# Performance work log

Measured on AMD Instinct MI355X. Metric: run time of the kernel, lower is better.

## Reference

```python
import jax, jax.numpy as jnp
import numpy as np

# Static ragged segment lengths (batch index column of `indices` is built to match).
COUNTS = (3072, 4096, 2048, 3584, 2560, 4096, 3072, 2048)
OFFSETS = np.concatenate([[0], np.cumsum(COUNTS)])  # static, jit-safe
N = int(OFFSETS[-1])
C_IN = 256
C_OUT = 256


def setup_inputs() -> dict:
    key = jax.random.key(0)
    kf, kq, kk, kv, kbq, kbk, kbv, kidx = jax.random.split(key, 8)
    features = jax.random.normal(kf, (N, C_IN), dtype=jnp.float32)
    # indices[:,0] = batch id (sorted, ragged counts); remaining cols = spatial coords.
    batch_col = jnp.asarray(np.repeat(np.arange(len(COUNTS)), COUNTS), dtype=jnp.int32)
    spatial = jax.random.randint(kidx, (N, 3), 0, 1024, dtype=jnp.int32)
    indices = jnp.concatenate([batch_col[:, None], spatial], axis=1)
    s = 1.0 / np.sqrt(C_IN)
    Wq = jax.random.normal(kq, (C_OUT, C_IN), dtype=jnp.float32) * s
    Wk = jax.random.normal(kk, (C_OUT, C_IN), dtype=jnp.float32) * s
    Wv = jax.random.normal(kv, (C_OUT, C_IN), dtype=jnp.float32) * s
    bq = jax.random.normal(kbq, (C_OUT,), dtype=jnp.float32) * 0.01
    bk = jax.random.normal(kbk, (C_OUT,), dtype=jnp.float32) * 0.01
    bv = jax.random.normal(kbv, (C_OUT,), dtype=jnp.float32) * 0.01
    return {"features": features, "indices": indices,
            "Wq": Wq, "bq": bq, "Wk": Wk, "bk": bk, "Wv": Wv, "bv": bv}


def reference(features, indices, Wq, bq, Wk, bk, Wv, bv):
    # Linear layers commute with the ragged split, so project once globally.
    q = features @ Wq.T + bq  # [N, C_OUT]
    k = features @ Wk.T + bk
    v = features @ Wv.T + bv
    outs = []
    for i in range(len(COUNTS)):  # small fixed set of ragged segments (static sizes)
        s, e = int(OFFSETS[i]), int(OFFSETS[i + 1])
        qi, ki, vi = q[s:e], k[s:e], v[s:e]  # [n_i, C]
        attn = jax.nn.softmax(qi @ ki.T, axis=-1)  # [n_i, n_i]
        outs.append(attn @ vi)
    return jnp.concatenate(outs, axis=0)  # [N, C_OUT]
```

## Files before the change

### kernel.cpp

```cpp
#include <hip/hip_runtime.h>


typedef _Float16 f16x8 __attribute__((ext_vector_type(8)));
typedef _Float16 f16x4 __attribute__((ext_vector_type(4)));
typedef _Float16 f16x2 __attribute__((ext_vector_type(2)));
typedef float    f32x4 __attribute__((ext_vector_type(4)));
typedef unsigned int u32;

#define MFMA(a,b,c) __builtin_amdgcn_mfma_f32_16x16x32_f16((a),(b),(c),0,0,0)

typedef __attribute__((address_space(1))) const u32 gu32_t;
typedef __attribute__((address_space(3))) u32 lu32_t;

__device__ __forceinline__ void gll16(const void* g, void* l) {
  __builtin_amdgcn_global_load_lds((gu32_t*)g, (lu32_t*)l, 16, 0, 0);
}
#define VMCNT(n) asm volatile("s_waitcnt vmcnt(" #n ")" ::: "memory")
#define BAR() __builtin_amdgcn_s_barrier()

__constant__ int c_off[9] = {0, 3072, 7168, 9216, 12800, 15360, 19456, 22528, 24576};

static constexpr int NTOK = 24576;
static constexpr int C    = 256;

__global__ __launch_bounds__(256) void wsplit_kernel(
    const float* __restrict__ Wq, const float* __restrict__ Wk, const float* __restrict__ Wv,
    _Float16* __restrict__ Whi, _Float16* __restrict__ Wlo)
{
  int idx = blockIdx.x * 256 + threadIdx.x;
  int mat = idx >> 16;
  int r   = idx & 65535;
  const float* W = (mat == 0) ? Wq : (mat == 1) ? Wk : Wv;
  float v = W[r];
  _Float16 h = (_Float16)v;
  Whi[idx] = h;
  Wlo[idx] = (_Float16)(v - (float)h);
}

__global__ __launch_bounds__(256) void proj_kernel(
    const float* __restrict__ X,
    const float* __restrict__ bq, const float* __restrict__ bk, const float* __restrict__ bv,
    const _Float16* __restrict__ Whi, const _Float16* __restrict__ Wlo,
    float* __restrict__ Qf, _Float16* __restrict__ Kh, _Float16* __restrict__ Vt)
{
  __shared__ _Float16 wl[2][2][16][256];

  const int tid  = threadIdx.x;
  const int w    = tid >> 6;
  const int lane = tid & 63;
  const int l15  = lane & 15;
  const int lg   = lane >> 4;
  const int t0   = blockIdx.x * 64 + w * 16;

  f16x8 xhi[8], xlo[8];
  {
    const float* src = X + (size_t)(t0 + l15) * C + lg * 8;
    #pragma unroll
    for (int kk = 0; kk < 8; ++kk) {
      float4 a = *(const float4*)(src + kk * 32);
      float4 b = *(const float4*)(src + kk * 32 + 4);
      float v[8] = {a.x, a.y, a.z, a.w, b.x, b.y, b.z, b.w};
      f16x8 h, l;
      #pragma unroll
      for (int j = 0; j < 8; ++j) {
        _Float16 hi = (_Float16)v[j];
        h[j] = hi;
        l[j] = (_Float16)(v[j] - (float)hi);
      }
      xhi[kk] = h;
      xlo[kk] = l;
    }
  }

  int soff[4];
  const _Float16* sbase[4];
  #pragma unroll
  for (int i = 0; i < 4; ++i) {
    int g = w * 256 + i * 64 + lane;
    int col = (g >> 5) & 15, p = g & 31;
    int c = (p & 24) | ((p ^ col) & 7);
    soff[i] = col * 256 + c * 8;
    sbase[i] = (g >> 9) ? Wlo : Whi;
  }

  int koff[8];
  {
    const int pm = l15 & 7;
    #pragma unroll
    for (int kk = 0; kk < 8; ++kk) {
      int cch = kk * 4 + lg;
      int p = (cch & 24) | ((cch ^ pm) & 7);
      koff[kk] = l15 * 512 + p * 16;
    }
  }

  auto stage = [&](int buf, int j) {
    const int rowbase = (j >> 4) * 256 + (j & 15) * 16;
    char* dst = (char*)&wl[buf][0][0][0] + (w * 256) * 16;
    #pragma unroll
    for (int i = 0; i < 4; ++i)
      gll16(sbase[i] + (size_t)rowbase * 256 + soff[i], dst + i * 1024);
  };

  stage(0, 0);
  stage(1, 1);
  VMCNT(4);
  BAR();

  #pragma unroll 1
  for (int j = 0; j < 48; ++j) {
    const int buf = j & 1;
    const char* bh_base = (const char*)&wl[buf][0][0][0];
    const char* bl_base = (const char*)&wl[buf][1][0][0];
    f32x4 acc = {0.f, 0.f, 0.f, 0.f};
    const int mat = j >> 4;
    if (mat < 2) {
      #pragma unroll
      for (int kk = 0; kk < 8; ++kk) {
        f16x8 bh = *(const f16x8*)(bh_base + koff[kk]);
        f16x8 bl = *(const f16x8*)(bl_base + koff[kk]);
        acc = MFMA(xhi[kk], bh, acc);
        acc = MFMA(xlo[kk], bh, acc);
        acc = MFMA(xhi[kk], bl, acc);
      }
    } else {
      #pragma unroll
      for (int kk = 0; kk < 8; ++kk) {
        f16x8 bh = *(const f16x8*)(bh_base + koff[kk]);
        acc = MFMA(xhi[kk], bh, acc);
      }
    }

    const int cg = (j & 15) * 16 + l15;
    const float bias = ((mat == 0) ? bq : (mat == 1) ? bk : bv)[cg];
    const int tok0 = t0 + lg * 4;
    if (mat == 0) {
      #pragma unroll
      for (int r = 0; r < 4; ++r)
        Qf[(size_t)(tok0 + r) * C + cg] = acc[r] + bias;
    } else if (mat == 1) {
      #pragma unroll
      for (int r = 0; r < 4; ++r)
        Kh[(size_t)(tok0 + r) * C + cg] = (_Float16)(acc[r] + bias);
    } else {
      f16x4 v4;
      #pragma unroll
      for (int r = 0; r < 4; ++r) v4[r] = (_Float16)(acc[r] + bias);
      *(f16x4*)(Vt + (size_t)cg * NTOK + tok0) = v4;
    }

    BAR();
    int jn = j + 2;
    if (jn >= 48) jn -= 48;
    stage(buf, jn);
    VMCNT(4);
    BAR();
  }
}

__global__ __launch_bounds__(256) void attn_kernel(
    const float* __restrict__ Qf, const _Float16* __restrict__ Kh,
    const _Float16* __restrict__ Vt, float* __restrict__ Out)
{
  __shared__ _Float16 k_lds[2][32][256];
  __shared__ _Float16 v_lds[2][256][32];
  __shared__ _Float16 p_lds[4][16][40];

  const int tid  = threadIdx.x;
  const int w    = tid >> 6;
  const int lane = tid & 63;
  const int l15  = lane & 15;
  const int lg   = lane >> 4;

  const int bid = blockIdx.x;
  const int qrow0 = ((bid & 7) * 48 + (bid >> 3)) * 64;

  int seg = 0;
  #pragma unroll
  for (int i = 1; i < 8; ++i)
    if (qrow0 >= c_off[i]) seg = i;
  const int s0 = c_off[seg];
  const int nt = (c_off[seg + 1] - s0) >> 5;

  f16x8 qhi[8], qlo[8];
  {
    const float* src = Qf + (size_t)(qrow0 + w * 16 + l15) * C + lg * 8;
    #pragma unroll
    for (int kk = 0; kk < 8; ++kk) {
      float4 a = *(const float4*)(src + kk * 32);
      float4 b = *(const float4*)(src + kk * 32 + 4);
      float v[8] = {a.x, a.y, a.z, a.w, b.x, b.y, b.z, b.w};
      f16x8 h, l;
      #pragma unroll
      for (int j = 0; j < 8; ++j) {
        _Float16 hi = (_Float16)v[j];
        h[j] = hi;
        l[j] = (_Float16)(v[j] - (float)hi);
      }
      qhi[kk] = h;
      qlo[kk] = l;
    }
  }

  int kso[4], vso[4];
  #pragma unroll
  for (int i = 0; i < 4; ++i) {
    int d = w * 256 + i * 64 + lane;
    { int r = d >> 5, p = d & 31;
      int c = (p & 24) | ((p ^ r) & 7);
      kso[i] = r * 256 + c * 8; }
    { int r = d >> 2, pd = d & 3;
      int c = pd ^ ((r >> 1) & 3);
      vso[i] = r * NTOK + c * 8; }
  }

  int koff[8];
  {
    const int pm = l15 & 7;
    #pragma unroll
    for (int kk = 0; kk < 8; ++kk) {
      int cch = kk * 4 + lg;
      int p = (cch & 24) | ((cch ^ pm) & 7);
      koff[kk] = l15 * 512 + p * 16;
    }
  }
  const int vrd = l15 * 64 + ((lg ^ ((l15 >> 1) & 3)) << 4);

  auto stageK = [&](int buf, int kv) {
    const _Float16* ks = Kh + (size_t)(s0 + kv) * C;
    char* kd = (char*)&k_lds[buf][0][0] + w * 4096;
    #pragma unroll
    for (int i = 0; i < 4; ++i) gll16(ks + kso[i], kd + i * 1024);
  };
  auto stageV = [&](int buf, int kv) {
    const _Float16* vs = Vt + (s0 + kv);
    char* vd = (char*)&v_lds[buf][0][0] + w * 4096;
    #pragma unroll
    for (int i = 0; i < 4; ++i) gll16(vs + vso[i], vd + i * 1024);
  };

  stageK(0, 0);
  stageV(0, 0);
  VMCNT(0);
  BAR();

  f32x4 o[16];
  #pragma unroll
  for (int db = 0; db < 16; ++db) o[db] = (f32x4){0.f, 0.f, 0.f, 0.f};
  float m_ = -1e30f;
  float ls = 0.f;

  #pragma unroll 1
  for (int t = 0; t < nt; ++t) {
    const int buf = t & 1;
    const int kvn = (t + 1 < nt) ? (t + 1) << 5 : 0;
    stageK(buf ^ 1, kvn);
    stageV(buf ^ 1, kvn);

    const char* kb = (const char*)&k_lds[buf][0][0];
    f32x4 s0v = {0.f, 0.f, 0.f, 0.f};
    f32x4 s1v = {0.f, 0.f, 0.f, 0.f};
    #pragma unroll
    for (int kk = 0; kk < 8; ++kk) {
      f16x8 b0 = *(const f16x8*)(kb + koff[kk]);
      f16x8 b1 = *(const f16x8*)(kb + koff[kk] + 8192);
      s0v = MFMA(b0, qhi[kk], s0v);
      s1v = MFMA(b1, qhi[kk], s1v);
      s0v = MFMA(b0, qlo[kk], s0v);
      s1v = MFMA(b1, qlo[kk], s1v);
    }

    float pmax = fmaxf(fmaxf(fmaxf(s0v[0], s0v[1]), fmaxf(s0v[2], s0v[3])),
                       fmaxf(fmaxf(s1v[0], s1v[1]), fmaxf(s1v[2], s1v[3])));
    pmax = fmaxf(pmax, __shfl_xor(pmax, 16));
    pmax = fmaxf(pmax, __shfl_xor(pmax, 32));

    const bool need = !__all(pmax <= m_ + 8.f);
    float scale = 1.f;
    if (need) {
      const float mn = fmaxf(m_, pmax);
      scale = __expf(m_ - mn);
      m_ = mn;
    }
    #pragma unroll
    for (int r = 0; r < 4; ++r) {
      s0v[r] = __expf(s0v[r] - m_);
      s1v[r] = __expf(s1v[r] - m_);
    }
    float rs = (s0v[0] + s0v[1]) + (s0v[2] + s0v[3]) +
               (s1v[0] + s1v[1]) + (s1v[2] + s1v[3]);
    rs += __shfl_xor(rs, 16);
    rs += __shfl_xor(rs, 32);
    ls = ls * scale + rs;

    {
      f16x2 a = {(_Float16)s0v[0], (_Float16)s0v[1]};
      f16x2 b = {(_Float16)s0v[2], (_Float16)s0v[3]};
      f16x2 c = {(_Float16)s1v[0], (_Float16)s1v[1]};
      f16x2 d = {(_Float16)s1v[2], (_Float16)s1v[3]};
      *(f16x2*)&p_lds[w][l15][lg * 4]      = a;
      *(f16x2*)&p_lds[w][l15][lg * 4 + 2]  = b;
      *(f16x2*)&p_lds[w][l15][16 + lg * 4]     = c;
      *(f16x2*)&p_lds[w][l15][16 + lg * 4 + 2] = d;
    }

    if (need) {
      float s4[4];
      #pragma unroll
      for (int r = 0; r < 4; ++r) s4[r] = __shfl(scale, lg * 4 + r);
      #pragma unroll
      for (int db = 0; db < 16; ++db) {
        #pragma unroll
        for (int r = 0; r < 4; ++r) o[db][r] *= s4[r];
      }
    }

    VMCNT(8);
    BAR();

    f16x8 pfrag = *(const f16x8*)&p_lds[w][l15][lg * 8];
    const char* vb = (const char*)&v_lds[buf][0][0] + vrd;
    #pragma unroll
    for (int db = 0; db < 16; ++db) {
      f16x8 vfrag = *(const f16x8*)(vb + db * 1024);
      o[db] = MFMA(pfrag, vfrag, o[db]);
    }

    VMCNT(4);
    BAR();
  }

  float l4[4];
  #pragma unroll
  for (int r = 0; r < 4; ++r) l4[r] = 1.f / __shfl(ls, lg * 4 + r);
  const int orow = qrow0 + w * 16 + lg * 4;
  #pragma unroll
  for (int db = 0; db < 16; ++db) {
    #pragma unroll
    for (int r = 0; r < 4; ++r) {
      Out[(size_t)(orow + r) * C + db * 16 + l15] = o[db][r] * l4[r];
    }
  }
}

extern "C" void kernel_launch(void* const* d_in, const int* in_sizes, int n_in,
                              void* d_out, int out_size, void* d_ws, size_t ws_size,
                              hipStream_t stream)
{
  const float* X  = (const float*)d_in[0];
  const float* Wq = (const float*)d_in[2];
  const float* bq = (const float*)d_in[3];
  const float* Wk = (const float*)d_in[4];
  const float* bk = (const float*)d_in[5];
  const float* Wv = (const float*)d_in[6];
  const float* bv = (const float*)d_in[7];
  float* Out = (float*)d_out;

  const size_t SZ = (size_t)NTOK * C;
  float*    Qf  = (float*)d_ws;
  _Float16* Kh  = (_Float16*)(Qf + SZ);
  _Float16* Vt  = Kh + SZ;
  _Float16* Whi = Vt + SZ;
  _Float16* Wlo = Whi + (size_t)3 * 65536;

  hipLaunchKernelGGL(wsplit_kernel, dim3(768), dim3(256), 0, stream,
                     Wq, Wk, Wv, Whi, Wlo);
  hipLaunchKernelGGL(proj_kernel, dim3(384), dim3(256), 0, stream,
                     X, bq, bk, bv, Whi, Wlo, Qf, Kh, Vt);
  hipLaunchKernelGGL(attn_kernel, dim3(384), dim3(256), 0, stream,
                     Qf, Kh, Vt, Out);
}
```

Before: 356.2 us.

## Drop split-fp16 precision emulation, restructure projection and attention kernels

```diff
diff --git a/kernel.cpp b/kernel.cpp
--- a/kernel.cpp
+++ b/kernel.cpp
@@ -15,7 +15,8 @@
 __device__ __forceinline__ void gll16(const void* g, void* l) {
   __builtin_amdgcn_global_load_lds((gu32_t*)g, (lu32_t*)l, 16, 0, 0);
 }
-#define VMCNT(n) asm volatile("s_waitcnt vmcnt(" #n ")" ::: "memory")
+#define VMCNT(n)  asm volatile("s_waitcnt vmcnt(" #n ")" ::: "memory")
+#define LGKMCNT0() asm volatile("s_waitcnt lgkmcnt(0)" ::: "memory")
 #define BAR() __builtin_amdgcn_s_barrier()
 
 __constant__ int c_off[9] = {0, 3072, 7168, 9216, 12800, 15360, 19456, 22528, 24576};
@@ -25,64 +26,55 @@
 
 __global__ __launch_bounds__(256) void wsplit_kernel(
     const float* __restrict__ Wq, const float* __restrict__ Wk, const float* __restrict__ Wv,
-    _Float16* __restrict__ Whi, _Float16* __restrict__ Wlo)
+    _Float16* __restrict__ Whi)
 {
   int idx = blockIdx.x * 256 + threadIdx.x;
   int mat = idx >> 16;
   int r   = idx & 65535;
   const float* W = (mat == 0) ? Wq : (mat == 1) ? Wk : Wv;
-  float v = W[r];
-  _Float16 h = (_Float16)v;
-  Whi[idx] = h;
-  Wlo[idx] = (_Float16)(v - (float)h);
+  Whi[idx] = (_Float16)W[r];
 }
 
 __global__ __launch_bounds__(256) void proj_kernel(
     const float* __restrict__ X,
     const float* __restrict__ bq, const float* __restrict__ bk, const float* __restrict__ bv,
-    const _Float16* __restrict__ Whi, const _Float16* __restrict__ Wlo,
-    float* __restrict__ Qf, _Float16* __restrict__ Kh, _Float16* __restrict__ Vt)
+    const _Float16* __restrict__ Whi,
+    _Float16* __restrict__ Qh, _Float16* __restrict__ Kh, _Float16* __restrict__ Vt)
 {
-  __shared__ _Float16 wl[2][2][16][256];
+  __shared__ _Float16 wl[4][2][16 * 256];
 
   const int tid  = threadIdx.x;
   const int w    = tid >> 6;
   const int lane = tid & 63;
   const int l15  = lane & 15;
   const int lg   = lane >> 4;
-  const int t0   = blockIdx.x * 64 + w * 16;
-
-  f16x8 xhi[8], xlo[8];
-  {
-    const float* src = X + (size_t)(t0 + l15) * C + lg * 8;
+  const int t0   = blockIdx.x * 32;
+
+  f16x8 xh[2][8];
+  #pragma unroll
+  for (int f = 0; f < 2; ++f) {
+    const float* src = X + (size_t)(t0 + f * 16 + l15) * C + lg * 8;
     #pragma unroll
     for (int kk = 0; kk < 8; ++kk) {
       float4 a = *(const float4*)(src + kk * 32);
       float4 b = *(const float4*)(src + kk * 32 + 4);
-      float v[8] = {a.x, a.y, a.z, a.w, b.x, b.y, b.z, b.w};
-      f16x8 h, l;
-      #pragma unroll
-      for (int j = 0; j < 8; ++j) {
-        _Float16 hi = (_Float16)v[j];
-        h[j] = hi;
-        l[j] = (_Float16)(v[j] - (float)hi);
-      }
-      xhi[kk] = h;
-      xlo[kk] = l;
-    }
-  }
-
-  int soff[4];
-  const _Float16* sbase[4];
-  #pragma unroll
-  for (int i = 0; i < 4; ++i) {
-    int g = w * 256 + i * 64 + lane;
-    int col = (g >> 5) & 15, p = g & 31;
+      f16x8 h;
+      h[0] = (_Float16)a.x; h[1] = (_Float16)a.y;
+      h[2] = (_Float16)a.z; h[3] = (_Float16)a.w;
+      h[4] = (_Float16)b.x; h[5] = (_Float16)b.y;
+      h[6] = (_Float16)b.z; h[7] = (_Float16)b.w;
+      xh[f][kk] = h;
+    }
+  }
+
+  int soff[8];
+  #pragma unroll
+  for (int i = 0; i < 8; ++i) {
+    int g = i * 64 + lane;
+    int col = g >> 5, p = g & 31;
     int c = (p & 24) | ((p ^ col) & 7);
     soff[i] = col * 256 + c * 8;
-    sbase[i] = (g >> 9) ? Wlo : Whi;
-  }
-
+  }
   int koff[8];
   {
     const int pm = l15 & 7;
@@ -96,75 +88,61 @@
 
   auto stage = [&](int buf, int j) {
     const int rowbase = (j >> 4) * 256 + (j & 15) * 16;
-    char* dst = (char*)&wl[buf][0][0][0] + (w * 256) * 16;
-    #pragma unroll
-    for (int i = 0; i < 4; ++i)
-      gll16(sbase[i] + (size_t)rowbase * 256 + soff[i], dst + i * 1024);
+    const _Float16* src0 = Whi + (size_t)rowbase * 256;
+    char* dst = (char*)&wl[w][buf][0];
+    #pragma unroll
+    for (int i = 0; i < 8; ++i)
+      gll16(src0 + soff[i], dst + i * 1024);
   };
 
-  stage(0, 0);
-  stage(1, 1);
-  VMCNT(4);
-  BAR();
+  stage(0, w);
+  stage(1, w + 4);
 
   #pragma unroll 1
-  for (int j = 0; j < 48; ++j) {
-    const int buf = j & 1;
-    const char* bh_base = (const char*)&wl[buf][0][0][0];
-    const char* bl_base = (const char*)&wl[buf][1][0][0];
-    f32x4 acc = {0.f, 0.f, 0.f, 0.f};
+  for (int i = 0; i < 12; ++i) {
+    const int j = w + i * 4;
+    if (i < 11) { VMCNT(8); } else { VMCNT(0); }
+    const char* bb = (const char*)&wl[w][i & 1][0];
+    f32x4 acc0 = {0.f, 0.f, 0.f, 0.f};
+    f32x4 acc1 = {0.f, 0.f, 0.f, 0.f};
+    #pragma unroll
+    for (int kk = 0; kk < 8; ++kk) {
+      f16x8 bh = *(const f16x8*)(bb + koff[kk]);
+      acc0 = MFMA(xh[0][kk], bh, acc0);
+      acc1 = MFMA(xh[1][kk], bh, acc1);
+    }
+
     const int mat = j >> 4;
-    if (mat < 2) {
-      #pragma unroll
-      for (int kk = 0; kk < 8; ++kk) {
-        f16x8 bh = *(const f16x8*)(bh_base + koff[kk]);
-        f16x8 bl = *(const f16x8*)(bl_base + koff[kk]);
-        acc = MFMA(xhi[kk], bh, acc);
-        acc = MFMA(xlo[kk], bh, acc);
-        acc = MFMA(xhi[kk], bl, acc);
+    const int cg  = (j & 15) * 16 + l15;
+    const float bias = ((mat == 0) ? bq : (mat == 1) ? bk : bv)[cg];
+    #pragma unroll
+    for (int f = 0; f < 2; ++f) {
+      f32x4 acc = f ? acc1 : acc0;
+      const int tok0 = t0 + f * 16 + lg * 4;
+      if (mat == 2) {
+        f16x4 v4;
+        #pragma unroll
+        for (int r = 0; r < 4; ++r) v4[r] = (_Float16)(acc[r] + bias);
+        *(f16x4*)(Vt + (size_t)cg * NTOK + tok0) = v4;
+      } else {
+        _Float16* P = (mat == 0) ? Qh : Kh;
+        #pragma unroll
+        for (int r = 0; r < 4; ++r)
+          P[(size_t)(tok0 + r) * C + cg] = (_Float16)(acc[r] + bias);
       }
-    } else {
-      #pragma unroll
-      for (int kk = 0; kk < 8; ++kk) {
-        f16x8 bh = *(const f16x8*)(bh_base + koff[kk]);
-        acc = MFMA(xhi[kk], bh, acc);
-      }
-    }
-
-    const int cg = (j & 15) * 16 + l15;
-    const float bias = ((mat == 0) ? bq : (mat == 1) ? bk : bv)[cg];
-    const int tok0 = t0 + lg * 4;
-    if (mat == 0) {
-      #pragma unroll
-      for (int r = 0; r < 4; ++r)
-        Qf[(size_t)(tok0 + r) * C + cg] = acc[r] + bias;
-    } else if (mat == 1) {
-      #pragma unroll
-      for (int r = 0; r < 4; ++r)
-        Kh[(size_t)(tok0 + r) * C + cg] = (_Float16)(acc[r] + bias);
-    } else {
-      f16x4 v4;
-      #pragma unroll
-      for (int r = 0; r < 4; ++r) v4[r] = (_Float16)(acc[r] + bias);
-      *(f16x4*)(Vt + (size_t)cg * NTOK + tok0) = v4;
-    }
-
-    BAR();
-    int jn = j + 2;
-    if (jn >= 48) jn -= 48;
-    stage(buf, jn);
-    VMCNT(4);
-    BAR();
-  }
-}
-
-__global__ __launch_bounds__(256) void attn_kernel(
-    const float* __restrict__ Qf, const _Float16* __restrict__ Kh,
+    }
+
+    LGKMCNT0();
+    if (i < 10) stage(i & 1, w + (i + 2) * 4);
+  }
+}
+
+__global__ __launch_bounds__(128, 2) void attn_kernel(
+    const _Float16* __restrict__ Qh, const _Float16* __restrict__ Kh,
     const _Float16* __restrict__ Vt, float* __restrict__ Out)
 {
-  __shared__ _Float16 k_lds[2][32][256];
-  __shared__ _Float16 v_lds[2][256][32];
-  __shared__ _Float16 p_lds[4][16][40];
+  __shared__ _Float16 k_lds[2][32 * 256];
+  __shared__ _Float16 p_lds[2][16][40];
 
   const int tid  = threadIdx.x;
   const int w    = tid >> 6;
@@ -173,7 +151,7 @@
   const int lg   = lane >> 4;
 
   const int bid = blockIdx.x;
-  const int qrow0 = ((bid & 7) * 48 + (bid >> 3)) * 64;
+  const int qrow0 = ((bid & 7) * 96 + (bid >> 3)) * 32;
 
   int seg = 0;
   #pragma unroll
@@ -182,38 +160,21 @@
   const int s0 = c_off[seg];
   const int nt = (c_off[seg + 1] - s0) >> 5;
 
-  f16x8 qhi[8], qlo[8];
+  f16x8 qf[8];
   {
-    const float* src = Qf + (size_t)(qrow0 + w * 16 + l15) * C + lg * 8;
-    #pragma unroll
-    for (int kk = 0; kk < 8; ++kk) {
-      float4 a = *(const float4*)(src + kk * 32);
-      float4 b = *(const float4*)(src + kk * 32 + 4);
-      float v[8] = {a.x, a.y, a.z, a.w, b.x, b.y, b.z, b.w};
-      f16x8 h, l;
-      #pragma unroll
-      for (int j = 0; j < 8; ++j) {
-        _Float16 hi = (_Float16)v[j];
-        h[j] = hi;
-        l[j] = (_Float16)(v[j] - (float)hi);
-      }
-      qhi[kk] = h;
-      qlo[kk] = l;
-    }
-  }
-
-  int kso[4], vso[4];
-  #pragma unroll
-  for (int i = 0; i < 4; ++i) {
-    int d = w * 256 + i * 64 + lane;
-    { int r = d >> 5, p = d & 31;
-      int c = (p & 24) | ((p ^ r) & 7);
-      kso[i] = r * 256 + c * 8; }
-    { int r = d >> 2, pd = d & 3;
-      int c = pd ^ ((r >> 1) & 3);
-      vso[i] = r * NTOK + c * 8; }
-  }
-
+    const _Float16* src = Qh + (size_t)(qrow0 + w * 16 + l15) * C + lg * 8;
+    #pragma unroll
+    for (int kk = 0; kk < 8; ++kk) qf[kk] = *(const f16x8*)(src + kk * 32);
+  }
+
+  int kso[8];
+  #pragma unroll
+  for (int i = 0; i < 8; ++i) {
+    int g = w * 512 + i * 64 + lane;
+    int r = g >> 5, p = g & 31;
+    int c = (p & 24) | ((p ^ r) & 7);
+    kso[i] = r * 256 + c * 8;
+  }
   int koff[8];
   {
     const int pm = l15 & 7;
@@ -224,24 +185,23 @@
       koff[kk] = l15 * 512 + p * 16;
     }
   }
-  const int vrd = l15 * 64 + ((lg ^ ((l15 >> 1) & 3)) << 4);
+
+  const _Float16* vbase = Vt + (size_t)l15 * NTOK + s0 + lg * 8;
 
   auto stageK = [&](int buf, int kv) {
     const _Float16* ks = Kh + (size_t)(s0 + kv) * C;
-    char* kd = (char*)&k_lds[buf][0][0] + w * 4096;
-    #pragma unroll
-    for (int i = 0; i < 4; ++i) gll16(ks + kso[i], kd + i * 1024);
+    char* kd = (char*)&k_lds[buf][0] + w * 8192;
+    #pragma unroll
+    for (int i = 0; i < 8; ++i) gll16(ks + kso[i], kd + i * 1024);
   };
-  auto stageV = [&](int buf, int kv) {
-    const _Float16* vs = Vt + (s0 + kv);
-    char* vd = (char*)&v_lds[buf][0][0] + w * 4096;
-    #pragma unroll
-    for (int i = 0; i < 4; ++i) gll16(vs + vso[i], vd + i * 1024);
-  };
+
+  f16x8 vf[16];
 
   stageK(0, 0);
-  stageV(0, 0);
-  VMCNT(0);
+  #pragma unroll
+  for (int db = 0; db < 16; ++db)
+    vf[db] = *(const f16x8*)(vbase + (size_t)db * (16 * NTOK));
+  VMCNT(16);
   BAR();
 
   f32x4 o[16];
@@ -255,19 +215,16 @@
     const int buf = t & 1;
     const int kvn = (t + 1 < nt) ? (t + 1) << 5 : 0;
     stageK(buf ^ 1, kvn);
-    stageV(buf ^ 1, kvn);
-
-    const char* kb = (const char*)&k_lds[buf][0][0];
+
+    const char* kb = (const char*)&k_lds[buf][0];
     f32x4 s0v = {0.f, 0.f, 0.f, 0.f};
     f32x4 s1v = {0.f, 0.f, 0.f, 0.f};
     #pragma unroll
     for (int kk = 0; kk < 8; ++kk) {
       f16x8 b0 = *(const f16x8*)(kb + koff[kk]);
       f16x8 b1 = *(const f16x8*)(kb + koff[kk] + 8192);
-      s0v = MFMA(b0, qhi[kk], s0v);
-      s1v = MFMA(b1, qhi[kk], s1v);
-      s0v = MFMA(b0, qlo[kk], s0v);
-      s1v = MFMA(b1, qlo[kk], s1v);
+      s0v = MFMA(b0, qf[kk], s0v);
+      s1v = MFMA(b1, qf[kk], s1v);
     }
 
     float pmax = fmaxf(fmaxf(fmaxf(s0v[0], s0v[1]), fmaxf(s0v[2], s0v[3])),
@@ -298,8 +255,8 @@
       f16x2 b = {(_Float16)s0v[2], (_Float16)s0v[3]};
       f16x2 c = {(_Float16)s1v[0], (_Float16)s1v[1]};
       f16x2 d = {(_Float16)s1v[2], (_Float16)s1v[3]};
-      *(f16x2*)&p_lds[w][l15][lg * 4]      = a;
-      *(f16x2*)&p_lds[w][l15][lg * 4 + 2]  = b;
+      *(f16x2*)&p_lds[w][l15][lg * 4]          = a;
+      *(f16x2*)&p_lds[w][l15][lg * 4 + 2]      = b;
       *(f16x2*)&p_lds[w][l15][16 + lg * 4]     = c;
       *(f16x2*)&p_lds[w][l15][16 + lg * 4 + 2] = d;
     }
@@ -315,18 +272,19 @@
       }
     }
 
-    VMCNT(8);
-    BAR();
-
     f16x8 pfrag = *(const f16x8*)&p_lds[w][l15][lg * 8];
-    const char* vb = (const char*)&v_lds[buf][0][0] + vrd;
-    #pragma unroll
-    for (int db = 0; db < 16; ++db) {
-      f16x8 vfrag = *(const f16x8*)(vb + db * 1024);
-      o[db] = MFMA(pfrag, vfrag, o[db]);
-    }
-
-    VMCNT(4);
+    #pragma unroll
+    for (int db = 0; db < 16; ++db)
+      o[db] = MFMA(pfrag, vf[db], o[db]);
+
+    {
+      const _Float16* vp = vbase + kvn;
+      #pragma unroll
+      for (int db = 0; db < 16; ++db)
+        vf[db] = *(const f16x8*)(vp + (size_t)db * (16 * NTOK));
+    }
+
+    VMCNT(16);
     BAR();
   }
 
@@ -357,16 +315,15 @@
   float* Out = (float*)d_out;
 
   const size_t SZ = (size_t)NTOK * C;
-  float*    Qf  = (float*)d_ws;
-  _Float16* Kh  = (_Float16*)(Qf + SZ);
+  _Float16* Qh  = (_Float16*)d_ws;
+  _Float16* Kh  = Qh + SZ;
   _Float16* Vt  = Kh + SZ;
   _Float16* Whi = Vt + SZ;
-  _Float16* Wlo = Whi + (size_t)3 * 65536;
 
   hipLaunchKernelGGL(wsplit_kernel, dim3(768), dim3(256), 0, stream,
-                     Wq, Wk, Wv, Whi, Wlo);
-  hipLaunchKernelGGL(proj_kernel, dim3(384), dim3(256), 0, stream,
-                     X, bq, bk, bv, Whi, Wlo, Qf, Kh, Vt);
-  hipLaunchKernelGGL(attn_kernel, dim3(384), dim3(256), 0, stream,
-                     Qf, Kh, Vt, Out);
-}
+                     Wq, Wk, Wv, Whi);
+  hipLaunchKernelGGL(proj_kernel, dim3(768), dim3(256), 0, stream,
+                     X, bq, bk, bv, Whi, Qh, Kh, Vt);
+  hipLaunchKernelGGL(attn_kernel, dim3(768), dim3(128), 0, stream,
+                     Qh, Kh, Vt, Out);
+}
```

Result: slower. 536.4 us (+50.6%).
